# Kernel optimization log

Hardware: AMD Instinct MI355X
Metric: run time of the kernel (lower is better)

Reference implementation:

```python
import jax, jax.numpy as jnp
import numpy as np

IMAGE_TOKEN = 32000
PAD_TOKEN = 0
IGNORE_INDEX = -100
PATCH = 14
B, S = 8, 1024
IMG = 336
VOCAB = 32064
D = 4096          # text embed_dim
DV = 1024         # vision hidden
N_LAYERS, N_EXPERTS, N_SHARED = 32, 8, 2
NP = (IMG // PATCH) ** 2          # 576 patches after dropping CLS
MAXE = (NP - 1) + S               # one <image> token per row -> 1599


def setup_inputs() -> dict:
    key = jax.random.key(0)
    ks = jax.random.split(key, 12)
    input_ids = jax.random.randint(ks[0], (B, S), 1, IMAGE_TOKEN)  # avoid pad(0) and image token
    input_ids = input_ids.at[:, 5].set(IMAGE_TOKEN)                # exactly one image token per row
    pixel_values = jax.random.normal(ks[1], (B, 3, IMG, IMG), jnp.float32)
    attention_mask = jnp.ones((B, S), jnp.int32)
    labels = jax.random.randint(ks[2], (B, S), 0, IMAGE_TOKEN)
    embed_table = jax.random.normal(ks[3], (VOCAB, D), jnp.float32) * 0.02
    cls_emb = jax.random.normal(ks[4], (DV,), jnp.float32) * 0.02
    patch_w = jax.random.normal(ks[5], (3 * PATCH * PATCH, DV), jnp.float32) * 0.02
    patch_b = jax.random.normal(ks[6], (DV,), jnp.float32) * 0.02
    proj_w1 = jax.random.normal(ks[7], (DV, D), jnp.float32) * 0.02
    proj_b1 = jax.random.normal(ks[8], (D,), jnp.float32) * 0.02
    proj_w2 = jax.random.normal(ks[9], (D, D), jnp.float32) * 0.02
    proj_b2 = jax.random.normal(ks[10], (D,), jnp.float32) * 0.02
    return dict(input_ids=input_ids, pixel_values=pixel_values, attention_mask=attention_mask,
                labels=labels, embed_table=embed_table, cls_emb=cls_emb, patch_w=patch_w,
                patch_b=patch_b, proj_w1=proj_w1, proj_b1=proj_b1, proj_w2=proj_w2, proj_b2=proj_b2)


def _vision_project(pixel_values, cls_emb, patch_w, patch_b, w1, b1, w2, b2):
    # Vision tower stub: patchify + linear patch embedding, CLS prepended,
    # then 'default' select strategy drops CLS, then 2-layer GELU projector.
    n = pixel_values.shape[0]
    g = IMG // PATCH
    x = pixel_values.reshape(n, 3, g, PATCH, g, PATCH)
    x = x.transpose(0, 2, 4, 1, 3, 5).reshape(n, g * g, 3 * PATCH * PATCH)
    h = x @ patch_w + patch_b                                   # [n, 576, DV]
    hidden = jnp.concatenate([jnp.broadcast_to(cls_emb, (n, 1, DV)), h], axis=1)  # [n, 577, DV]
    sel = hidden[:, 1:]                                          # drop CLS ('default')
    return jax.nn.gelu(sel @ w1 + b1) @ w2 + b2                  # [n, 576, D]


def _merge(image_features, inputs_embeds, input_ids, attention_mask, labels):
    b, s = input_ids.shape
    n, p, d = image_features.shape
    special = input_ids == IMAGE_TOKEN                           # [B,S]
    left_padding = jnp.sum(input_ids[:, -1] == PAD_TOKEN) == 0
    new_pos = jnp.cumsum(special.astype(jnp.int32) * (p - 1) + 1, axis=-1) - 1
    nb_pad = MAXE - 1 - new_pos[:, -1]
    new_pos = new_pos + jnp.where(left_padding, nb_pad[:, None], 0)
    pos_safe = jnp.where(special, MAXE, new_pos)                 # OOB index for image tokens -> dropped
    bi = jnp.arange(b)[:, None]
    final_emb = jnp.zeros((b, MAXE, d), inputs_embeds.dtype).at[bi, pos_safe].set(inputs_embeds, mode='drop')
    final_attn = jnp.zeros((b, MAXE), attention_mask.dtype).at[bi, pos_safe].set(attention_mask, mode='drop')
    final_labels = jnp.full((b, MAXE), IGNORE_INDEX, labels.dtype).at[bi, pos_safe].set(labels, mode='drop')
    img_ow = jnp.all(final_emb == 0, axis=-1)                    # slots never written by text
    img_ow = img_ow & (jnp.cumsum(img_ow.astype(jnp.int32), axis=-1) - 1 >= nb_pad[:, None])
    flat_mask = img_ow.reshape(-1)                               # [B*MAXE]
    rank = jnp.cumsum(flat_mask.astype(jnp.int32)) - 1           # row-major rank of each True slot
    img_flat = image_features.reshape(-1, d)                     # [n*p, D]
    gathered = img_flat[jnp.clip(rank, 0, img_flat.shape[0] - 1)]
    final_emb = jnp.where(flat_mask[:, None], gathered, final_emb.reshape(-1, d)).reshape(b, MAXE, d)
    final_attn = jnp.where(img_ow, jnp.ones_like(final_attn), final_attn)
    return final_emb, final_attn, final_labels


def reference(input_ids, pixel_values, attention_mask, labels, embed_table, cls_emb,
              patch_w, patch_b, proj_w1, proj_b1, proj_w2, proj_b2):
    inputs_embeds = embed_table[input_ids]                       # [B,S,D]
    image_features = _vision_project(pixel_values, cls_emb, patch_w, patch_b,
                                     proj_w1, proj_b1, proj_w2, proj_b2)
    final_emb, final_attn, final_labels = _merge(image_features, inputs_embeds,
                                                 input_ids, attention_mask, labels)
    # torch.empty buffers (uninitialized scratch) -> zeros for determinism
    router_logits = jnp.zeros((N_LAYERS, MAXE, N_EXPERTS), jnp.float32)
    shared_router_logits = jnp.zeros((N_LAYERS, MAXE, N_SHARED), jnp.float32)
    current_layer = jnp.int32(0)
    return (current_layer, final_emb, final_attn, final_labels, router_logits, shared_router_logits)
```

## Files before the change

kernel.cpp:

```cpp
#include <hip/hip_runtime.h>
#include <math.h>

#define B_ 8
#define S_ 1024
#define D_ 4096
#define DV_ 1024
#define NP_ 576
#define MAXE_ 1599
#define PK_ 588
#define KP_ 608
#define IMG_ 336
#define GRID_ 24
#define PATCH_ 14
#define IMAGE_TOKEN_ 32000
#define PAD_TOKEN_ 0
#define NLAYERS_ 32
#define NEXP_ 8
#define NSH_ 2

#define EMB_ELEMS ((size_t)B_ * MAXE_ * D_)
#define OFF_EMB   ((size_t)1)
#define OFF_ATTN  (OFF_EMB + EMB_ELEMS)
#define OFF_LAB   (OFF_ATTN + (size_t)B_ * MAXE_)
#define OFF_ROUTER (OFF_LAB + (size_t)B_ * MAXE_)
#define ROUTER_ELEMS ((size_t)NLAYERS_ * MAXE_ * (NEXP_ + NSH_))

typedef __bf16 bf16x8 __attribute__((ext_vector_type(8)));
typedef float  f32x4  __attribute__((ext_vector_type(4)));
typedef unsigned short ushort_t;

__device__ __forceinline__ unsigned short f2bf(float f) {
    unsigned u = __float_as_uint(f);
    u += 0x7fffu + ((u >> 16) & 1u);
    return (unsigned short)(u >> 16);
}

__device__ __forceinline__ float bf2f(unsigned short u) {
    return __uint_as_float((unsigned)u << 16);
}

__device__ __forceinline__ void async_copy16(const void* g, void* l) {
    __builtin_amdgcn_global_load_lds(
        (const __attribute__((address_space(1))) void*)g,
        (__attribute__((address_space(3))) void*)l, 16, 0, 0);
}

__global__ void fill_tail_kernel(float* __restrict__ out) {
    size_t i = (size_t)blockIdx.x * blockDim.x + threadIdx.x;
    if (i == 0) out[0] = 0.0f;
    for (size_t j = i; j < ROUTER_ELEMS; j += (size_t)gridDim.x * blockDim.x)
        out[OFF_ROUTER + j] = 0.0f;
}

__global__ __launch_bounds__(512) void merge_kernel(
    const int* __restrict__ input_ids, const int* __restrict__ attn_mask,
    const int* __restrict__ labels, float* __restrict__ out,
    int* __restrict__ src_index, int* __restrict__ img_pos)
{
    __shared__ int sh_nbpad[B_];
    __shared__ int sh_shift[B_];
    __shared__ int sh_nqual[B_];
    __shared__ int sh_leftpad;
    float* out_attn = out + OFF_ATTN;
    float* out_lab  = out + OFF_LAB;
    const int tid = threadIdx.x;

    for (int i = tid; i < B_ * MAXE_; i += blockDim.x) {
        src_index[i] = -1;
        out_attn[i] = 0.0f;
        out_lab[i] = -100.0f;
    }
    for (int i = tid; i < B_ * NP_; i += blockDim.x) img_pos[i] = -1;
    if (tid == 0) {
        int anypad = 0;
        for (int b = 0; b < B_; b++)
            if (input_ids[b * S_ + S_ - 1] == PAD_TOKEN_) anypad = 1;
        sh_leftpad = !anypad;
    }
    __syncthreads();

    const int wave = tid >> 6;
    const int lane = tid & 63;
    const unsigned long long below = (1ull << lane) - 1ull;

    if (wave < B_) {
        const int b = wave;
        int nspec = 0;
        for (int c = 0; c < S_; c += 64) {
            int id = input_ids[b * S_ + c + lane];
            nspec += __popcll(__ballot(id == IMAGE_TOKEN_));
        }
        int nb_pad = MAXE_ - S_ - (NP_ - 1) * nspec;
        int shift = sh_leftpad ? nb_pad : 0;
        int nholes = MAXE_ - (S_ - nspec);
        int nq = nholes - nb_pad; if (nq < 0) nq = 0;
        if (lane == 0) { sh_nbpad[b] = nb_pad; sh_shift[b] = shift; sh_nqual[b] = nq; }
        int carry = 0;
        for (int c = 0; c < S_; c += 64) {
            int t = c + lane;
            int id = input_ids[b * S_ + t];
            int spec = (id == IMAGE_TOKEN_);
            unsigned long long m = __ballot(spec);
            int nbefore = carry + __popcll(m & below);
            if (!spec) {
                int pos = t + (NP_ - 1) * nbefore + shift;
                if (pos >= 0 && pos < MAXE_) {
                    src_index[b * MAXE_ + pos] = t;
                    out_attn[b * MAXE_ + pos] = (float)attn_mask[b * S_ + t];
                    out_lab[b * MAXE_ + pos]  = (float)labels[b * S_ + t];
                }
            }
            carry += __popcll(m);
        }
    }
    __syncthreads();

    if (wave < B_) {
        const int b = wave;
        int offs = 0;
        for (int r = 0; r < b; r++) offs += sh_nqual[r];
        const int nb_pad = sh_nbpad[b];
        int hcarry = 0;
        for (int c = 0; c < MAXE_; c += 64) {
            int p = c + lane;
            int flag = 0;
            if (p < MAXE_) flag = (src_index[b * MAXE_ + p] == -1);
            unsigned long long m = __ballot(flag);
            int h = hcarry + __popcll(m & below);
            if (flag && h >= nb_pad) {
                int g = offs + (h - nb_pad);
                if (g > B_ * NP_ - 1) g = B_ * NP_ - 1;
                if (g < 0) g = 0;
                img_pos[g] = b * MAXE_ + p;
                src_index[b * MAXE_ + p] = -2;
                out_attn[b * MAXE_ + p] = 1.0f;
            }
            hcarry += __popcll(m);
        }
    }
}

__global__ void patchify_split_kernel(const float* __restrict__ pix,
                                      ushort_t* __restrict__ xh,
                                      ushort_t* __restrict__ xl)
{
    int i = blockIdx.x * blockDim.x + threadIdx.x;
    const int total = B_ * NP_ * KP_;
    if (i >= total) return;
    int q = i % KP_;
    int t = (i / KP_) % NP_;
    int n = i / (KP_ * NP_);
    float v = 0.0f;
    if (q < PK_) {
        int c = q / (PATCH_ * PATCH_);
        int r = q % (PATCH_ * PATCH_);
        int py = r / PATCH_, px = r % PATCH_;
        int gy = t / GRID_, gx = t % GRID_;
        v = pix[(((size_t)n * 3 + c) * IMG_ + gy * PATCH_ + py) * IMG_ + gx * PATCH_ + px];
    }
    ushort_t h = f2bf(v);
    xh[i] = h;
    xl[i] = f2bf(v - bf2f(h));
}

__global__ __launch_bounds__(256) void transpose_bf16_kernel(
    const float* __restrict__ src, ushort_t* __restrict__ dst, int R, int C)
{
    __shared__ float tile[32][33];
    int c0 = blockIdx.x * 32, r0 = blockIdx.y * 32;
    int tx = threadIdx.x & 31, ty = threadIdx.x >> 5;
    for (int i = ty; i < 32; i += 8)
        tile[i][tx] = src[(size_t)(r0 + i) * C + c0 + tx];
    __syncthreads();
    int j = threadIdx.x & 15;
    int k = threadIdx.x >> 4;
#pragma unroll
    for (int p = 0; p < 2; p++) {
        int i = k + p * 16;
        ushort2 v;
        v.x = f2bf(tile[2 * j][i]);
        v.y = f2bf(tile[2 * j + 1][i]);
        *(ushort2*)&dst[(size_t)(c0 + i) * R + r0 + 2 * j] = v;
    }
}

__global__ __launch_bounds__(256) void transpose_split_kernel(
    const float* __restrict__ src, ushort_t* __restrict__ dh,
    ushort_t* __restrict__ dl, int R, int C, int RP)
{
    __shared__ float tile[32][33];
    int c0 = blockIdx.x * 32, r0 = blockIdx.y * 32;
    int tx = threadIdx.x & 31, ty = threadIdx.x >> 5;
    for (int i = ty; i < 32; i += 8) {
        float v = 0.0f;
        if (r0 + i < R && c0 + tx < C) v = src[(size_t)(r0 + i) * C + c0 + tx];
        tile[i][tx] = v;
    }
    __syncthreads();
    for (int i = ty; i < 32; i += 8) {
        if (c0 + i < C && r0 + tx < RP) {
            float v = tile[tx][i];
            ushort_t h = f2bf(v);
            dh[(size_t)(c0 + i) * RP + r0 + tx] = h;
            dl[(size_t)(c0 + i) * RP + r0 + tx] = f2bf(v - bf2f(h));
        }
    }
}

__global__ __launch_bounds__(256) void mfma_gemm_split(
    const ushort_t* __restrict__ Ah, const ushort_t* __restrict__ Al,
    const ushort_t* __restrict__ Bth, const ushort_t* __restrict__ Btl,
    const float* __restrict__ bias, ushort_t* __restrict__ outb,
    int M, int N, int K)
{
    __shared__ ushort_t Ash[128 * 32];
    __shared__ ushort_t Asl[128 * 32];
    __shared__ ushort_t Bsh[128 * 32];
    __shared__ ushort_t Bsl[128 * 32];
    const int tid  = threadIdx.x;
    const int wave = tid >> 6;
    const int lane = tid & 63;
    const int l16  = lane & 15;
    const int quad = lane >> 4;
    const int wrow = (wave >> 1) * 64;
    const int wcol = (wave & 1) * 64;
    const int row0 = blockIdx.y * 128;
    const int col0 = blockIdx.x * 128;

    f32x4 acc[4][4];
#pragma unroll
    for (int i = 0; i < 4; i++)
#pragma unroll
        for (int j = 0; j < 4; j++) acc[i][j] = (f32x4)(0.0f);

    const int R0a = wave * 32;
    const int lr  = lane >> 2;
    const int lc  = (lane & 3) * 8;

    for (int k0 = 0; k0 < K; k0 += 32) {
#pragma unroll
        for (int i = 0; i < 2; i++) {
            int R0 = R0a + i * 16;
            size_t aoff = (size_t)(row0 + R0 + lr) * K + k0 + lc;
            size_t boff = (size_t)(col0 + R0 + lr) * K + k0 + lc;
            async_copy16(Ah  + aoff, &Ash[R0 * 32]);
            async_copy16(Al  + aoff, &Asl[R0 * 32]);
            async_copy16(Bth + boff, &Bsh[R0 * 32]);
            async_copy16(Btl + boff, &Bsl[R0 * 32]);
        }
        __syncthreads();

        bf16x8 ah[4], al[4], bh[4], bl[4];
#pragma unroll
        for (int mt = 0; mt < 4; mt++) {
            ah[mt] = *(const bf16x8*)&Ash[(wrow + mt * 16 + l16) * 32 + quad * 8];
            al[mt] = *(const bf16x8*)&Asl[(wrow + mt * 16 + l16) * 32 + quad * 8];
        }
#pragma unroll
        for (int nt = 0; nt < 4; nt++) {
            bh[nt] = *(const bf16x8*)&Bsh[(wcol + nt * 16 + l16) * 32 + quad * 8];
            bl[nt] = *(const bf16x8*)&Bsl[(wcol + nt * 16 + l16) * 32 + quad * 8];
        }
#pragma unroll
        for (int mt = 0; mt < 4; mt++)
#pragma unroll
            for (int nt = 0; nt < 4; nt++) {
                acc[mt][nt] = __builtin_amdgcn_mfma_f32_16x16x32_bf16(
                    ah[mt], bh[nt], acc[mt][nt], 0, 0, 0);
                acc[mt][nt] = __builtin_amdgcn_mfma_f32_16x16x32_bf16(
                    ah[mt], bl[nt], acc[mt][nt], 0, 0, 0);
                acc[mt][nt] = __builtin_amdgcn_mfma_f32_16x16x32_bf16(
                    al[mt], bh[nt], acc[mt][nt], 0, 0, 0);
            }
        __syncthreads();
    }

    float bv[4];
#pragma unroll
    for (int nt = 0; nt < 4; nt++) bv[nt] = bias[col0 + wcol + nt * 16 + l16];

#pragma unroll
    for (int mt = 0; mt < 4; mt++) {
#pragma unroll
        for (int r = 0; r < 4; r++) {
            int row = row0 + wrow + mt * 16 + quad * 4 + r;
            ushort_t* dst = outb + (size_t)row * N;
#pragma unroll
            for (int nt = 0; nt < 4; nt++) {
                int col = col0 + wcol + nt * 16 + l16;
                dst[col] = f2bf(acc[mt][nt][r] + bv[nt]);
            }
        }
    }
}

__global__ __launch_bounds__(256) void mfma_gemm_bt(
    const ushort_t* __restrict__ A, const ushort_t* __restrict__ Bt,
    const float* __restrict__ bias, ushort_t* __restrict__ outb,
    float* __restrict__ outf, const int* __restrict__ pos_map,
    int M, int N, int K, int mode)
{
    __shared__ ushort_t As[128 * 32];
    __shared__ ushort_t Bs[128 * 32];
    const int tid  = threadIdx.x;
    const int wave = tid >> 6;
    const int lane = tid & 63;
    const int l16  = lane & 15;
    const int quad = lane >> 4;
    const int wrow = (wave >> 1) * 64;
    const int wcol = (wave & 1) * 64;
    const int row0 = blockIdx.y * 128;
    const int col0 = blockIdx.x * 128;

    f32x4 acc[4][4];
#pragma unroll
    for (int i = 0; i < 4; i++)
#pragma unroll
        for (int j = 0; j < 4; j++) acc[i][j] = (f32x4)(0.0f);

    const int R0a = wave * 32;
    const int lr  = lane >> 2;
    const int lc  = (lane & 3) * 8;

    for (int k0 = 0; k0 < K; k0 += 32) {
#pragma unroll
        for (int i = 0; i < 2; i++) {
            int R0 = R0a + i * 16;
            const ushort_t* ga = A  + (size_t)(row0 + R0 + lr) * K + k0 + lc;
            const ushort_t* gb = Bt + (size_t)(col0 + R0 + lr) * K + k0 + lc;
            async_copy16(ga, &As[R0 * 32]);
            async_copy16(gb, &Bs[R0 * 32]);
        }
        __syncthreads();

        bf16x8 af[4], bf[4];
#pragma unroll
        for (int mt = 0; mt < 4; mt++)
            af[mt] = *(const bf16x8*)&As[(wrow + mt * 16 + l16) * 32 + quad * 8];
#pragma unroll
        for (int nt = 0; nt < 4; nt++)
            bf[nt] = *(const bf16x8*)&Bs[(wcol + nt * 16 + l16) * 32 + quad * 8];
#pragma unroll
        for (int mt = 0; mt < 4; mt++)
#pragma unroll
            for (int nt = 0; nt < 4; nt++)
                acc[mt][nt] = __builtin_amdgcn_mfma_f32_16x16x32_bf16(
                    af[mt], bf[nt], acc[mt][nt], 0, 0, 0);
        __syncthreads();
    }

    float bv[4];
#pragma unroll
    for (int nt = 0; nt < 4; nt++) bv[nt] = bias[col0 + wcol + nt * 16 + l16];

#pragma unroll
    for (int mt = 0; mt < 4; mt++) {
#pragma unroll
        for (int r = 0; r < 4; r++) {
            int row = row0 + wrow + mt * 16 + quad * 4 + r;
            if (mode == 2) {
                int orow = pos_map[row];
                if (orow < 0) continue;
#pragma unroll
                for (int nt = 0; nt < 4; nt++) {
                    int col = col0 + wcol + nt * 16 + l16;
                    outf[(size_t)orow * N + col] = acc[mt][nt][r] + bv[nt];
                }
            } else {
#pragma unroll
                for (int nt = 0; nt < 4; nt++) {
                    int col = col0 + wcol + nt * 16 + l16;
                    float x = acc[mt][nt][r] + bv[nt];
                    float u = 0.7978845608028654f * (x + 0.044715f * x * x * x);
                    x = x / (1.0f + __expf(-2.0f * u));
                    outb[(size_t)row * N + col] = f2bf(x);
                }
            }
        }
    }
}

__global__ __launch_bounds__(256) void scatter_text_kernel(
    const int* __restrict__ src_index, const int* __restrict__ input_ids,
    const float* __restrict__ embed, float* __restrict__ final_emb)
{
    int row = blockIdx.x;
    int src = src_index[row];
    if (src == -2) return;
    float4* dst = (float4*)(final_emb + (size_t)row * D_);
    if (src >= 0) {
        int b = row / MAXE_;
        int tok = input_ids[b * S_ + src];
        const float4* s = (const float4*)(embed + (size_t)tok * D_);
#pragma unroll
        for (int i = threadIdx.x; i < D_ / 4; i += 256) dst[i] = s[i];
    } else {
#pragma unroll
        for (int i = threadIdx.x; i < D_ / 4; i += 256)
            dst[i] = make_float4(0.f, 0.f, 0.f, 0.f);
    }
}

extern "C" void kernel_launch(void* const* d_in, const int* in_sizes, int n_in,
                              void* d_out, int out_size, void* d_ws, size_t ws_size,
                              hipStream_t stream)
{
    const int*   input_ids = (const int*)d_in[0];
    const float* pixel     = (const float*)d_in[1];
    const int*   attn      = (const int*)d_in[2];
    const int*   labels    = (const int*)d_in[3];
    const float* embed     = (const float*)d_in[4];
    const float* patch_w   = (const float*)d_in[6];
    const float* patch_b   = (const float*)d_in[7];
    const float* w1        = (const float*)d_in[8];
    const float* b1        = (const float*)d_in[9];
    const float* w2        = (const float*)d_in[10];
    const float* b2        = (const float*)d_in[11];
    float* out = (float*)d_out;

    char* w = (char*)d_ws;
    int* src_index = (int*)w;
    int* img_pos   = (int*)(w + 51200);
    ushort_t* xh   = (ushort_t*)(w + 51200 + 18432);
    ushort_t* xl   = xh  + (size_t)B_ * NP_ * KP_;
    ushort_t* pwh  = xl  + (size_t)B_ * NP_ * KP_;
    ushort_t* pwl  = pwh + (size_t)DV_ * KP_;
    ushort_t* hbuf = pwl + (size_t)DV_ * KP_;
    ushort_t* g1   = hbuf + (size_t)B_ * NP_ * DV_;
    ushort_t* w1t  = g1 + (size_t)B_ * NP_ * D_;
    ushort_t* w2t  = w1t + (size_t)D_ * DV_;

    fill_tail_kernel<<<2048, 256, 0, stream>>>(out);
    merge_kernel<<<1, 512, 0, stream>>>(input_ids, attn, labels, out, src_index, img_pos);

    {
        int total = B_ * NP_ * KP_;
        patchify_split_kernel<<<(total + 255) / 256, 256, 0, stream>>>(pixel, xh, xl);
    }
    transpose_split_kernel<<<dim3(DV_ / 32, KP_ / 32), 256, 0, stream>>>(
        patch_w, pwh, pwl, PK_, DV_, KP_);
    transpose_bf16_kernel<<<dim3(D_ / 32, DV_ / 32), 256, 0, stream>>>(w1, w1t, DV_, D_);
    transpose_bf16_kernel<<<dim3(D_ / 32, D_ / 32), 256, 0, stream>>>(w2, w2t, D_, D_);

    const int M = B_ * NP_;
    mfma_gemm_split<<<dim3(DV_ / 128, M / 128), 256, 0, stream>>>(
        xh, xl, pwh, pwl, patch_b, hbuf, M, DV_, KP_);
    mfma_gemm_bt<<<dim3(D_ / 128, M / 128), 256, 0, stream>>>(
        hbuf, w1t, b1, g1, nullptr, nullptr, M, D_, DV_, 1);
    mfma_gemm_bt<<<dim3(D_ / 128, M / 128), 256, 0, stream>>>(
        g1, w2t, b2, nullptr, out + OFF_EMB, img_pos, M, D_, D_, 2);

    scatter_text_kernel<<<B_ * MAXE_, 256, 0, stream>>>(src_index, input_ids, embed, out + OFF_EMB);
}
```

Baseline: 1.085 ms.

## Fuse prep kernels into one launch and move merge init to fill kernel

Merges the patchify, patch-weight split-transpose and two weight transpose kernels into a single kernel that dispatches on block index ranges, cutting three kernel launches. It also moves the initialization of src_index, attention, labels and img_pos from the single-block merge kernel into the grid-wide fill kernel, so that work is spread across many blocks instead of one. The fused kernel has branchy per-block roles, and its shared tile is allocated for all blocks.

```diff
diff --git a/kernel.cpp b/kernel.cpp
--- a/kernel.cpp
+++ b/kernel.cpp
@@ -45,11 +45,24 @@
         (__attribute__((address_space(3))) void*)l, 16, 0, 0);
 }
 
-__global__ void fill_tail_kernel(float* __restrict__ out) {
+__global__ void fill_tail_kernel(float* __restrict__ out,
+                                 int* __restrict__ src_index,
+                                 int* __restrict__ img_pos)
+{
     size_t i = (size_t)blockIdx.x * blockDim.x + threadIdx.x;
+    size_t stride = (size_t)gridDim.x * blockDim.x;
     if (i == 0) out[0] = 0.0f;
-    for (size_t j = i; j < ROUTER_ELEMS; j += (size_t)gridDim.x * blockDim.x)
+    for (size_t j = i; j < ROUTER_ELEMS; j += stride)
         out[OFF_ROUTER + j] = 0.0f;
+    float* out_attn = out + OFF_ATTN;
+    float* out_lab  = out + OFF_LAB;
+    for (size_t j = i; j < (size_t)B_ * MAXE_; j += stride) {
+        src_index[j] = -1;
+        out_attn[j] = 0.0f;
+        out_lab[j] = -100.0f;
+    }
+    for (size_t j = i; j < (size_t)B_ * NP_; j += stride)
+        img_pos[j] = -1;
 }
 
 __global__ __launch_bounds__(512) void merge_kernel(
@@ -65,12 +78,6 @@
     float* out_lab  = out + OFF_LAB;
     const int tid = threadIdx.x;
 
-    for (int i = tid; i < B_ * MAXE_; i += blockDim.x) {
-        src_index[i] = -1;
-        out_attn[i] = 0.0f;
-        out_lab[i] = -100.0f;
-    }
-    for (int i = tid; i < B_ * NP_; i += blockDim.x) img_pos[i] = -1;
     if (tid == 0) {
         int anypad = 0;
         for (int b = 0; b < B_; b++)
@@ -140,37 +147,78 @@
     }
 }
 
-__global__ void patchify_split_kernel(const float* __restrict__ pix,
-                                      ushort_t* __restrict__ xh,
-                                      ushort_t* __restrict__ xl)
-{
-    int i = blockIdx.x * blockDim.x + threadIdx.x;
-    const int total = B_ * NP_ * KP_;
-    if (i >= total) return;
-    int q = i % KP_;
-    int t = (i / KP_) % NP_;
-    int n = i / (KP_ * NP_);
-    float v = 0.0f;
-    if (q < PK_) {
-        int c = q / (PATCH_ * PATCH_);
-        int r = q % (PATCH_ * PATCH_);
-        int py = r / PATCH_, px = r % PATCH_;
-        int gy = t / GRID_, gx = t % GRID_;
-        v = pix[(((size_t)n * 3 + c) * IMG_ + gy * PATCH_ + py) * IMG_ + gx * PATCH_ + px];
-    }
-    ushort_t h = f2bf(v);
-    xh[i] = h;
-    xl[i] = f2bf(v - bf2f(h));
-}
-
-__global__ __launch_bounds__(256) void transpose_bf16_kernel(
-    const float* __restrict__ src, ushort_t* __restrict__ dst, int R, int C)
+#define NPATCH_BLOCKS ((B_ * NP_ * KP_ + 255) / 256)
+#define NTS_BLOCKS    ((DV_ / 32) * (KP_ / 32))
+#define NT1_BLOCKS    ((D_ / 32) * (DV_ / 32))
+#define NT2_BLOCKS    ((D_ / 32) * (D_ / 32))
+#define PREP_BLOCKS   (NPATCH_BLOCKS + NTS_BLOCKS + NT1_BLOCKS + NT2_BLOCKS)
+
+__global__ __launch_bounds__(256) void prep_fused_kernel(
+    const float* __restrict__ pix, ushort_t* __restrict__ xh, ushort_t* __restrict__ xl,
+    const float* __restrict__ patch_w, ushort_t* __restrict__ pwh, ushort_t* __restrict__ pwl,
+    const float* __restrict__ w1, ushort_t* __restrict__ w1t,
+    const float* __restrict__ w2, ushort_t* __restrict__ w2t)
 {
     __shared__ float tile[32][33];
-    int c0 = blockIdx.x * 32, r0 = blockIdx.y * 32;
+    int bid = blockIdx.x;
+
+    if (bid < NPATCH_BLOCKS) {
+        int i = bid * 256 + threadIdx.x;
+        if (i >= B_ * NP_ * KP_) return;
+        int q = i % KP_;
+        int t = (i / KP_) % NP_;
+        int n = i / (KP_ * NP_);
+        float v = 0.0f;
+        if (q < PK_) {
+            int c = q / (PATCH_ * PATCH_);
+            int r = q % (PATCH_ * PATCH_);
+            int py = r / PATCH_, px = r % PATCH_;
+            int gy = t / GRID_, gx = t % GRID_;
+            v = pix[(((size_t)n * 3 + c) * IMG_ + gy * PATCH_ + py) * IMG_ + gx * PATCH_ + px];
+        }
+        ushort_t h = f2bf(v);
+        xh[i] = h;
+        xl[i] = f2bf(v - bf2f(h));
+        return;
+    }
+    bid -= NPATCH_BLOCKS;
+
+    if (bid < NTS_BLOCKS) {
+        int bx = bid & 31;
+        int by = bid >> 5;
+        int c0 = bx * 32, r0 = by * 32;
+        int tx = threadIdx.x & 31, ty = threadIdx.x >> 5;
+        for (int i = ty; i < 32; i += 8) {
+            float v = 0.0f;
+            if (r0 + i < PK_) v = patch_w[(size_t)(r0 + i) * DV_ + c0 + tx];
+            tile[i][tx] = v;
+        }
+        __syncthreads();
+        for (int i = ty; i < 32; i += 8) {
+            if (r0 + tx < KP_) {
+                float v = tile[tx][i];
+                ushort_t h = f2bf(v);
+                pwh[(size_t)(c0 + i) * KP_ + r0 + tx] = h;
+                pwl[(size_t)(c0 + i) * KP_ + r0 + tx] = f2bf(v - bf2f(h));
+            }
+        }
+        return;
+    }
+    bid -= NTS_BLOCKS;
+
+    const float* src; ushort_t* dst; int R;
+    if (bid < NT1_BLOCKS) {
+        src = w1; dst = w1t; R = DV_;
+    } else {
+        bid -= NT1_BLOCKS;
+        src = w2; dst = w2t; R = D_;
+    }
+    int bx = bid & 127;
+    int by = bid >> 7;
+    int c0 = bx * 32, r0 = by * 32;
     int tx = threadIdx.x & 31, ty = threadIdx.x >> 5;
     for (int i = ty; i < 32; i += 8)
-        tile[i][tx] = src[(size_t)(r0 + i) * C + c0 + tx];
+        tile[i][tx] = src[(size_t)(r0 + i) * D_ + c0 + tx];
     __syncthreads();
     int j = threadIdx.x & 15;
     int k = threadIdx.x >> 4;
@@ -181,29 +229,6 @@
         v.x = f2bf(tile[2 * j][i]);
         v.y = f2bf(tile[2 * j + 1][i]);
         *(ushort2*)&dst[(size_t)(c0 + i) * R + r0 + 2 * j] = v;
-    }
-}
-
-__global__ __launch_bounds__(256) void transpose_split_kernel(
-    const float* __restrict__ src, ushort_t* __restrict__ dh,
-    ushort_t* __restrict__ dl, int R, int C, int RP)
-{
-    __shared__ float tile[32][33];
-    int c0 = blockIdx.x * 32, r0 = blockIdx.y * 32;
-    int tx = threadIdx.x & 31, ty = threadIdx.x >> 5;
-    for (int i = ty; i < 32; i += 8) {
-        float v = 0.0f;
-        if (r0 + i < R && c0 + tx < C) v = src[(size_t)(r0 + i) * C + c0 + tx];
-        tile[i][tx] = v;
-    }
-    __syncthreads();
-    for (int i = ty; i < 32; i += 8) {
-        if (c0 + i < C && r0 + tx < RP) {
-            float v = tile[tx][i];
-            ushort_t h = f2bf(v);
-            dh[(size_t)(c0 + i) * RP + r0 + tx] = h;
-            dl[(size_t)(c0 + i) * RP + r0 + tx] = f2bf(v - bf2f(h));
-        }
     }
 }
 
@@ -430,17 +455,11 @@
     ushort_t* w1t  = g1 + (size_t)B_ * NP_ * D_;
     ushort_t* w2t  = w1t + (size_t)D_ * DV_;
 
-    fill_tail_kernel<<<2048, 256, 0, stream>>>(out);
+    fill_tail_kernel<<<2048, 256, 0, stream>>>(out, src_index, img_pos);
     merge_kernel<<<1, 512, 0, stream>>>(input_ids, attn, labels, out, src_index, img_pos);
 
-    {
-        int total = B_ * NP_ * KP_;
-        patchify_split_kernel<<<(total + 255) / 256, 256, 0, stream>>>(pixel, xh, xl);
-    }
-    transpose_split_kernel<<<dim3(DV_ / 32, KP_ / 32), 256, 0, stream>>>(
-        patch_w, pwh, pwl, PK_, DV_, KP_);
-    transpose_bf16_kernel<<<dim3(D_ / 32, DV_ / 32), 256, 0, stream>>>(w1, w1t, DV_, D_);
-    transpose_bf16_kernel<<<dim3(D_ / 32, D_ / 32), 256, 0, stream>>>(w2, w2t, D_, D_);
+    prep_fused_kernel<<<PREP_BLOCKS, 256, 0, stream>>>(
+        pixel, xh, xl, patch_w, pwh, pwl, w1, w1t, w2, w2t);
 
     const int M = B_ * NP_;
     mfma_gemm_split<<<dim3(DV_ / 128, M / 128), 256, 0, stream>>>(
```

New measurement: 1.071 ms. About the same (-1.3%).
